# Kernel optimization log

Hardware: AMD Instinct MI355X
Metric: run time of the kernel (lower is better)

## Reference

```python
import jax, jax.numpy as jnp
import numpy as np

HEADS = 4
C_HEAD = 32


def setup_inputs() -> dict:
    key = jax.random.key(0)
    k1, k2, k3 = jax.random.split(key, 3)
    c_in = 256
    c_hid = HEADS * C_HEAD  # 128
    x = jax.random.normal(k1, (4, c_in, 64, 64), dtype=jnp.float32)
    # 1x1 conv weights stored as [out, in]
    w_qkv = jax.random.normal(k2, (3 * c_hid, c_in), dtype=jnp.float32) * (c_in ** -0.5)
    w_out = jax.random.normal(k3, (c_in, c_hid), dtype=jnp.float32) * (c_hid ** -0.5)
    b_out = jnp.zeros((c_in,), dtype=jnp.float32)
    return {"x": x, "w_qkv": w_qkv, "w_out": w_out, "b_out": b_out}


def reference(x, w_qkv, w_out, b_out):
    b, c, h, w = x.shape
    scale = C_HEAD ** -0.5
    # 1x1 conv == channel matmul
    qkv = jnp.einsum('bchw,oc->bohw', x, w_qkv)  # [b, 3*c_hid, h, w]
    q, k, v = jnp.split(qkv, 3, axis=1)
    # b (heads c_head) x y -> b heads c_head (x y)
    def to_heads(t):
        return t.reshape(b, HEADS, C_HEAD, h * w)
    q, k, v = to_heads(q) * scale, to_heads(k), to_heads(v)
    sim = jnp.einsum('bhci,bhcj->bhij', q, k)  # [b, heads, N, N]
    sim = sim - jax.lax.stop_gradient(jnp.max(sim, axis=-1, keepdims=True))
    attn = jax.nn.softmax(sim, axis=-1)
    out = jnp.einsum('bhij,bhcj->bhic', attn, v)  # [b, heads, N, c_head]
    # b h (x y) c -> b (h c) x y
    out = out.transpose(0, 1, 3, 2).reshape(b, HEADS * C_HEAD, h, w)
    out = jnp.einsum('bchw,oc->bohw', out, w_out) + b_out[None, :, None, None]
    return out
```

## Files before the change

kernel.cpp:

```cpp
#include <hip/hip_runtime.h>
#include <hip/hip_bf16.h>
#include <cstdint>
#include <cstddef>

#define NB 4
#define CIN 256
#define CHID 128
#define HEADS 4
#define CHEAD 32
#define NPOS 4096
#define BH 16
#define NTOT 16384
#define QKV_O 384
#define QSCALE_LOG2E 0.2550348229f

typedef float f32x4 __attribute__((ext_vector_type(4)));
typedef float f32x16 __attribute__((ext_vector_type(16)));
typedef short s16x8 __attribute__((ext_vector_type(8)));

static __device__ __forceinline__ unsigned short f2bf(float f) {
    union { float f; unsigned u; } v; v.f = f;
    unsigned r = v.u + 0x7FFFu + ((v.u >> 16) & 1u);
    return (unsigned short)(r >> 16);
}

static __device__ __forceinline__ unsigned int pk2bf(float a, float b) {
    union { __hip_bfloat162 h; unsigned int u; } c;
    c.h = __float22bfloat162_rn(float2{a, b});
    return c.u;
}

static __device__ __forceinline__ void plswap(unsigned& a, unsigned& b) {
#if __has_builtin(__builtin_amdgcn_permlane32_swap)
    auto r = __builtin_amdgcn_permlane32_swap((int)a, (int)b, false, false);
    a = (unsigned)r[0];
    b = (unsigned)r[1];
#else
    int hh = (threadIdx.x >> 5) & 1;
    unsigned ta = (unsigned)__shfl_xor((int)a, 32);
    unsigned tb = (unsigned)__shfl_xor((int)b, 32);
    unsigned na = hh ? tb : a;
    unsigned nb = hh ? b : ta;
    a = na; b = nb;
#endif
}

static __device__ __forceinline__ s16x8 mk8(unsigned a, unsigned b, unsigned c, unsigned d) {
    union { unsigned u[4]; s16x8 v; } x;
    x.u[0] = a; x.u[1] = b; x.u[2] = c; x.u[3] = d;
    return x.v;
}

static __device__ __forceinline__ void async_cp16(const void* g, void* l) {
    __builtin_amdgcn_global_load_lds((const __attribute__((address_space(1))) unsigned int*)g,
                                     (__attribute__((address_space(3))) unsigned int*)l, 16, 0, 0);
}

#define MFMA32(a, b, c) __builtin_amdgcn_mfma_f32_32x32x16_bf16(a, b, c, 0, 0, 0)

__global__ void k_convert_w(const float* __restrict__ wqkv, const float* __restrict__ wout,
                            unsigned short* __restrict__ wqkv_bf, unsigned short* __restrict__ wout_bf) {
    int i = blockIdx.x * 256 + threadIdx.x;
    if (i < QKV_O * CIN) wqkv_bf[i] = f2bf(wqkv[i]);
    if (i < CIN * CHID)  wout_bf[i]  = f2bf(wout[i]);
}

__global__ __launch_bounds__(256) void k_transpose_x(const float* __restrict__ x,
                                                     unsigned short* __restrict__ xT) {
    __shared__ float tile[32][33];
    const int ntiles = NPOS / 32;
    const int ctiles = CIN / 32;
    int b   = blockIdx.x / (ntiles * ctiles);
    int rem = blockIdx.x % (ntiles * ctiles);
    int ct = rem / ntiles;
    int nt = rem % ntiles;
    int c0 = ct * 32, n0 = nt * 32;
    int tc = threadIdx.x / 32;
    int tn = threadIdx.x % 32;
    const float* xb = x + (size_t)b * CIN * NPOS;
#pragma unroll
    for (int it = 0; it < 4; ++it) {
        int c = tc + it * 8;
        tile[c][tn] = xb[(size_t)(c0 + c) * NPOS + n0 + tn];
    }
    __syncthreads();
    unsigned short* xTb = xT + (size_t)b * NPOS * CIN;
#pragma unroll
    for (int it = 0; it < 4; ++it) {
        int n = tc + it * 8;
        xTb[(size_t)(n0 + n) * CIN + c0 + tn] = f2bf(tile[tn][n]);
    }
}

__global__ __launch_bounds__(256, 4) void k_qkv(const unsigned short* __restrict__ wq,
                                                const unsigned short* __restrict__ xT,
                                                unsigned short* __restrict__ Q,
                                                unsigned short* __restrict__ K,
                                                unsigned short* __restrict__ V) {
    __shared__ __align__(16) unsigned char smem[2 * 12288];
    int mt = blockIdx.x % 3;
    int nt = blockIdx.x / 3;
    int wid = threadIdx.x >> 6, lane = threadIdx.x & 63;
    int quad = lane >> 4, low4 = lane & 15;
    int o0 = mt * 128, n0 = nt * 64;
    int lb = lane * 16;

    const unsigned short* srcA0 = wq + (size_t)(o0 + wid * 32 + low4) * CIN + quad * 8;
    const unsigned short* srcA1 = srcA0 + 16 * CIN;
    const unsigned short* srcB  = xT + (size_t)(n0 + wid * 16 + low4) * CIN + quad * 8;
    int dA0 = wid * 2048, dA1 = dA0 + 1024, dB = 8192 + wid * 1024;

    async_cp16(srcA0, smem + dA0 + lb);
    async_cp16(srcA1, smem + dA1 + lb);
    async_cp16(srcB,  smem + dB  + lb);
    __syncthreads();

    f32x4 acc[2][4] = {};
    for (int c = 0; c < 8; ++c) {
        if (c < 7) {
            unsigned char* nxt = smem + ((c + 1) & 1) * 12288;
            async_cp16(srcA0 + (c + 1) * 32, nxt + dA0 + lb);
            async_cp16(srcA1 + (c + 1) * 32, nxt + dA1 + lb);
            async_cp16(srcB  + (c + 1) * 32, nxt + dB  + lb);
        }
        const unsigned char* cur = smem + (c & 1) * 12288;
        s16x8 a0 = *(const s16x8*)(cur + wid * 2048 + lb);
        s16x8 a1 = *(const s16x8*)(cur + wid * 2048 + 1024 + lb);
#pragma unroll
        for (int j = 0; j < 4; ++j) {
            s16x8 bj = *(const s16x8*)(cur + 8192 + j * 1024 + lb);
            acc[0][j] = __builtin_amdgcn_mfma_f32_16x16x32_bf16(a0, bj, acc[0][j], 0, 0, 0);
            acc[1][j] = __builtin_amdgcn_mfma_f32_16x16x32_bf16(a1, bj, acc[1][j], 0, 0, 0);
        }
        __syncthreads();
    }

#pragma unroll
    for (int i = 0; i < 2; ++i) {
        int ob = o0 + wid * 32 + i * 16 + quad * 4;
#pragma unroll
        for (int j = 0; j < 4; ++j) {
            int nG = n0 + j * 16 + low4;
            int b = nG >> 12, n = nG & 4095;
            f32x4 v = acc[i][j];
            if (ob < 128) {
                int head = ob >> 5, ch = ob & 31;
                unsigned long long d =
                    (unsigned long long)pk2bf(v[0] * QSCALE_LOG2E, v[1] * QSCALE_LOG2E) |
                    ((unsigned long long)pk2bf(v[2] * QSCALE_LOG2E, v[3] * QSCALE_LOG2E) << 32);
                *(unsigned long long*)(Q + ((size_t)(b * 4 + head) * NPOS + n) * 32 + ch) = d;
            } else if (ob < 256) {
                int o2 = ob - 128; int head = o2 >> 5, ch = o2 & 31;
                unsigned long long d =
                    (unsigned long long)pk2bf(v[0], v[1]) |
                    ((unsigned long long)pk2bf(v[2], v[3]) << 32);
                *(unsigned long long*)(K + ((size_t)(b * 4 + head) * NPOS + n) * 32 + ch) = d;
            } else {
#pragma unroll
                for (int r = 0; r < 4; ++r) {
                    int o2 = ob + r - 256; int head = o2 >> 5, ch = o2 & 31;
                    V[((size_t)((b * 4 + head) * 32 + ch)) * NPOS + n] = f2bf(v[r]);
                }
            }
        }
    }
}

__global__ __launch_bounds__(256, 2) void k_attn(const unsigned short* __restrict__ Q,
                                                 const unsigned short* __restrict__ K,
                                                 const unsigned short* __restrict__ V,
                                                 unsigned short* __restrict__ attnO) {
    __shared__ __align__(16) unsigned char smem[2 * 16384];
    int bh = blockIdx.x & 15;
    int qt = blockIdx.x >> 4;
    int wid = threadIdx.x >> 6, lane = threadIdx.x & 63;
    int q5 = lane & 31, h = lane >> 5;
    int qg = wid & 1, kh = wid >> 1;
    int q0 = qt * 128 + qg * 64;
    int khk = kh * 2048;

    const unsigned short* Qp  = Q + (size_t)bh * NPOS * 32;
    const unsigned short* Kbh = K + (size_t)bh * NPOS * 32;
    const unsigned short* Vbh = V + (size_t)bh * 32 * NPOS;

    s16x8 bq00 = *(const s16x8*)(Qp + (size_t)(q0 + q5) * 32 + h * 8);
    s16x8 bq01 = *(const s16x8*)(Qp + (size_t)(q0 + q5) * 32 + 16 + h * 8);
    s16x8 bq10 = *(const s16x8*)(Qp + (size_t)(q0 + 32 + q5) * 32 + h * 8);
    s16x8 bq11 = *(const s16x8*)(Qp + (size_t)(q0 + 32 + q5) * 32 + 16 + h * 8);

    const unsigned short* sK = Kbh + (size_t)q5 * 32 + h * 8;
    const unsigned short* sV = Vbh + (size_t)q5 * NPOS + h * 8;
    unsigned char* wbase0 = smem + kh * 8192;
    unsigned char* wbase1 = smem + 16384 + kh * 8192;

    auto stage = [&](int bufi, int k0) {
        unsigned char* wb = bufi ? wbase1 : wbase0;
        if (qg == 0) {
            const unsigned short* p = sK + (size_t)k0 * 32;
            async_cp16(p,        wb);
            async_cp16(p + 16,   wb + 1024);
            async_cp16(p + 1024, wb + 2048);
            async_cp16(p + 1040, wb + 3072);
        } else {
            const unsigned short* p = sV + k0;
            async_cp16(p,      wb + 4096);
            async_cp16(p + 16, wb + 5120);
            async_cp16(p + 32, wb + 6144);
            async_cp16(p + 48, wb + 7168);
        }
    };

    f32x16 oT0 = {}, oT1 = {};
    float lsum0 = 0.0f, lsum1 = 0.0f;
    const int lby = lane * 16;

    stage(0, khk);
    __syncthreads();

#pragma unroll 1
    for (int it = 0; it < 32; ++it) {
        if (it + 1 < 32) stage((it + 1) & 1, khk + (it + 1) * 64);
        const unsigned char* kb = smem + (it & 1) * 16384 + kh * 8192;
#pragma unroll
        for (int t = 0; t < 2; ++t) {
            s16x8 ak0 = *(const s16x8*)(kb + t * 2048 + lby);
            s16x8 ak1 = *(const s16x8*)(kb + t * 2048 + 1024 + lby);
            f32x16 s0 = {}, s1 = {};
            s0 = MFMA32(ak0, bq00, s0); s0 = MFMA32(ak1, bq01, s0);
            s1 = MFMA32(ak0, bq10, s1); s1 = MFMA32(ak1, bq11, s1);
            unsigned p0[8], p1[8];
#pragma unroll
            for (int i = 0; i < 8; ++i) {
                float a0 = __builtin_amdgcn_exp2f(s0[2 * i]);
                float a1 = __builtin_amdgcn_exp2f(s0[2 * i + 1]);
                float b0 = __builtin_amdgcn_exp2f(s1[2 * i]);
                float b1 = __builtin_amdgcn_exp2f(s1[2 * i + 1]);
                lsum0 += a0 + a1;
                lsum1 += b0 + b1;
                p0[i] = pk2bf(a0, a1);
                p1[i] = pk2bf(b0, b1);
            }
            plswap(p0[0], p0[2]); plswap(p0[1], p0[3]);
            plswap(p0[4], p0[6]); plswap(p0[5], p0[7]);
            plswap(p1[0], p1[2]); plswap(p1[1], p1[3]);
            plswap(p1[4], p1[6]); plswap(p1[5], p1[7]);
            s16x8 bp0lo = mk8(p0[0], p0[1], p0[2], p0[3]);
            s16x8 bp0hi = mk8(p0[4], p0[5], p0[6], p0[7]);
            s16x8 bp1lo = mk8(p1[0], p1[1], p1[2], p1[3]);
            s16x8 bp1hi = mk8(p1[4], p1[5], p1[6], p1[7]);

            s16x8 av0 = *(const s16x8*)(kb + 4096 + (2 * t) * 1024 + lby);
            s16x8 av1 = *(const s16x8*)(kb + 4096 + (2 * t + 1) * 1024 + lby);
            oT0 = MFMA32(av0, bp0lo, oT0); oT0 = MFMA32(av1, bp0hi, oT0);
            oT1 = MFMA32(av0, bp1lo, oT1); oT1 = MFMA32(av1, bp1hi, oT1);
        }
        __syncthreads();
    }

    lsum0 += __shfl_xor(lsum0, 32);
    lsum1 += __shfl_xor(lsum1, 32);

    float* area = (float*)smem + qg * 2176;
    if (kh) {
#pragma unroll
        for (int j = 0; j < 4; ++j) {
            *(f32x4*)(area + j * 256 + lane * 4) =
                f32x4{oT0[4 * j], oT0[4 * j + 1], oT0[4 * j + 2], oT0[4 * j + 3]};
            *(f32x4*)(area + 1024 + j * 256 + lane * 4) =
                f32x4{oT1[4 * j], oT1[4 * j + 1], oT1[4 * j + 2], oT1[4 * j + 3]};
        }
        area[2048 + lane * 2]     = lsum0;
        area[2048 + lane * 2 + 1] = lsum1;
    }
    __syncthreads();
    if (!kh) {
        lsum0 += area[2048 + lane * 2];
        lsum1 += area[2048 + lane * 2 + 1];
        float inv0 = 1.0f / lsum0, inv1 = 1.0f / lsum1;
        int b = bh >> 2, head = bh & 3;
        int n0 = q0 + q5, n1 = q0 + 32 + q5;
        unsigned short* base0 = attnO + ((size_t)(b * NPOS + n0)) * CHID + head * 32 + 4 * h;
        unsigned short* base1 = attnO + ((size_t)(b * NPOS + n1)) * CHID + head * 32 + 4 * h;
#pragma unroll
        for (int j = 0; j < 4; ++j) {
            f32x4 r0 = *(const f32x4*)(area + j * 256 + lane * 4);
            f32x4 r1 = *(const f32x4*)(area + 1024 + j * 256 + lane * 4);
            unsigned long long d0 =
                (unsigned long long)pk2bf((oT0[4 * j] + r0[0]) * inv0, (oT0[4 * j + 1] + r0[1]) * inv0) |
                ((unsigned long long)pk2bf((oT0[4 * j + 2] + r0[2]) * inv0, (oT0[4 * j + 3] + r0[3]) * inv0) << 32);
            *(unsigned long long*)(base0 + 8 * j) = d0;
            unsigned long long d1 =
                (unsigned long long)pk2bf((oT1[4 * j] + r1[0]) * inv1, (oT1[4 * j + 1] + r1[1]) * inv1) |
                ((unsigned long long)pk2bf((oT1[4 * j + 2] + r1[2]) * inv1, (oT1[4 * j + 3] + r1[3]) * inv1) << 32);
            *(unsigned long long*)(base1 + 8 * j) = d1;
        }
    }
}

__global__ __launch_bounds__(256, 4) void k_out(const unsigned short* __restrict__ wo,
                                                const unsigned short* __restrict__ attnO,
                                                const float* __restrict__ bias,
                                                float* __restrict__ out) {
    __shared__ __align__(16) unsigned char smem[2 * 12288];
    int mt = blockIdx.x & 1;
    int nt = blockIdx.x >> 1;
    int wid = threadIdx.x >> 6, lane = threadIdx.x & 63;
    int quad = lane >> 4, low4 = lane & 15;
    int o0 = mt * 128, n0 = nt * 64;
    int lb = lane * 16;

    const unsigned short* srcA0 = wo + (size_t)(o0 + wid * 32 + low4) * CHID + quad * 8;
    const unsigned short* srcA1 = srcA0 + 16 * CHID;
    const unsigned short* srcB  = attnO + (size_t)(n0 + wid * 16 + low4) * CHID + quad * 8;
    int dA0 = wid * 2048, dA1 = dA0 + 1024, dB = 8192 + wid * 1024;

    async_cp16(srcA0, smem + dA0 + lb);
    async_cp16(srcA1, smem + dA1 + lb);
    async_cp16(srcB,  smem + dB  + lb);
    __syncthreads();

    f32x4 acc[2][4] = {};
    for (int c = 0; c < 4; ++c) {
        if (c < 3) {
            unsigned char* nxt = smem + ((c + 1) & 1) * 12288;
            async_cp16(srcA0 + (c + 1) * 32, nxt + dA0 + lb);
            async_cp16(srcA1 + (c + 1) * 32, nxt + dA1 + lb);
            async_cp16(srcB  + (c + 1) * 32, nxt + dB  + lb);
        }
        const unsigned char* cur = smem + (c & 1) * 12288;
        s16x8 a0 = *(const s16x8*)(cur + wid * 2048 + lb);
        s16x8 a1 = *(const s16x8*)(cur + wid * 2048 + 1024 + lb);
#pragma unroll
        for (int j = 0; j < 4; ++j) {
            s16x8 bj = *(const s16x8*)(cur + 8192 + j * 1024 + lb);
            acc[0][j] = __builtin_amdgcn_mfma_f32_16x16x32_bf16(a0, bj, acc[0][j], 0, 0, 0);
            acc[1][j] = __builtin_amdgcn_mfma_f32_16x16x32_bf16(a1, bj, acc[1][j], 0, 0, 0);
        }
        __syncthreads();
    }

#pragma unroll
    for (int i = 0; i < 2; ++i) {
        int ob = o0 + wid * 32 + i * 16 + quad * 4;
#pragma unroll
        for (int j = 0; j < 4; ++j) {
            int nG = n0 + j * 16 + low4;
            int b = nG >> 12, n = nG & 4095;
#pragma unroll
            for (int r = 0; r < 4; ++r) {
                int o = ob + r;
                out[((size_t)(b * CIN + o)) * NPOS + n] = acc[i][j][r] + bias[o];
            }
        }
    }
}

extern "C" void kernel_launch(void* const* d_in, const int* in_sizes, int n_in,
                              void* d_out, int out_size, void* d_ws, size_t ws_size,
                              hipStream_t stream) {
    const float* x    = (const float*)d_in[0];
    const float* wqkv = (const float*)d_in[1];
    const float* wout = (const float*)d_in[2];
    const float* bout = (const float*)d_in[3];
    float* out = (float*)d_out;

    unsigned short* Q       = (unsigned short*)d_ws;
    unsigned short* K       = Q + (size_t)BH * NPOS * 32;
    unsigned short* V       = K + (size_t)BH * NPOS * 32;
    unsigned short* attnO   = V + (size_t)BH * 32 * NPOS;
    unsigned short* xT      = attnO + (size_t)NTOT * CHID;
    unsigned short* wqkv_bf = xT + (size_t)NTOT * CIN;
    unsigned short* wout_bf = wqkv_bf + QKV_O * CIN;

    k_convert_w<<<(QKV_O * CIN + 255) / 256, 256, 0, stream>>>(wqkv, wout, wqkv_bf, wout_bf);
    k_transpose_x<<<NB * (CIN / 32) * (NPOS / 32), 256, 0, stream>>>(x, xT);
    k_qkv<<<3 * (NTOT / 64), 256, 0, stream>>>(wqkv_bf, xT, Q, K, V);
    k_attn<<<(NPOS / 128) * BH, 256, 0, stream>>>(Q, K, V, attnO);
    k_out<<<2 * (NTOT / 64), 256, 0, stream>>>(wout_bf, attnO, bout, out);
}
```

Baseline: 153.6 us.

## Split attention keys across more waves, fuse prep kernels, stage V stores via LDS

The attention kernel now launches 512 threads per block, so the key range is split four ways instead of two. The partial outputs from the extra waves are reduced through a larger 64KB shared buffer. The weight conversion and x transpose are merged into one launch, and the V-tile stores in the qkv kernel are transposed through LDS so they can be written as coalesced 16-byte vectors. The row-sum accumulator is also split into two chains to shorten the dependency. The trade-offs are a larger LDS footprint per attention block, which may cap occupancy, and an extra cross-wave reduction step.

```diff
diff --git a/kernel.cpp b/kernel.cpp
--- a/kernel.cpp
+++ b/kernel.cpp
@@ -58,15 +58,19 @@
 
 #define MFMA32(a, b, c) __builtin_amdgcn_mfma_f32_32x32x16_bf16(a, b, c, 0, 0, 0)
 
-__global__ void k_convert_w(const float* __restrict__ wqkv, const float* __restrict__ wout,
-                            unsigned short* __restrict__ wqkv_bf, unsigned short* __restrict__ wout_bf) {
-    int i = blockIdx.x * 256 + threadIdx.x;
-    if (i < QKV_O * CIN) wqkv_bf[i] = f2bf(wqkv[i]);
-    if (i < CIN * CHID)  wout_bf[i]  = f2bf(wout[i]);
-}
-
-__global__ __launch_bounds__(256) void k_transpose_x(const float* __restrict__ x,
-                                                     unsigned short* __restrict__ xT) {
+#define TBLOCKS (NB * (CIN / 32) * (NPOS / 32))
+__global__ __launch_bounds__(256) void k_prep(const float* __restrict__ x,
+                                              unsigned short* __restrict__ xT,
+                                              const float* __restrict__ wqkv,
+                                              const float* __restrict__ wout,
+                                              unsigned short* __restrict__ wqkv_bf,
+                                              unsigned short* __restrict__ wout_bf) {
+    if (blockIdx.x >= TBLOCKS) {
+        int i = (blockIdx.x - TBLOCKS) * 256 + threadIdx.x;
+        if (i < QKV_O * CIN) wqkv_bf[i] = f2bf(wqkv[i]);
+        if (i < CIN * CHID)  wout_bf[i] = f2bf(wout[i]);
+        return;
+    }
     __shared__ float tile[32][33];
     const int ntiles = NPOS / 32;
     const int ctiles = CIN / 32;
@@ -135,49 +139,62 @@
         __syncthreads();
     }
 
-#pragma unroll
-    for (int i = 0; i < 2; ++i) {
-        int ob = o0 + wid * 32 + i * 16 + quad * 4;
-#pragma unroll
-        for (int j = 0; j < 4; ++j) {
-            int nG = n0 + j * 16 + low4;
-            int b = nG >> 12, n = nG & 4095;
-            f32x4 v = acc[i][j];
-            if (ob < 128) {
-                int head = ob >> 5, ch = ob & 31;
+    if (mt < 2) {
+        unsigned short* dst = (mt == 0) ? Q : K;
+        float sc = (mt == 0) ? QSCALE_LOG2E : 1.0f;
+#pragma unroll
+        for (int i = 0; i < 2; ++i) {
+            int ol = wid * 32 + i * 16 + quad * 4;
+            int head = ol >> 5, ch = ol & 31;
+#pragma unroll
+            for (int j = 0; j < 4; ++j) {
+                int nG = n0 + j * 16 + low4;
+                int b = nG >> 12, n = nG & 4095;
+                f32x4 v = acc[i][j];
                 unsigned long long d =
-                    (unsigned long long)pk2bf(v[0] * QSCALE_LOG2E, v[1] * QSCALE_LOG2E) |
-                    ((unsigned long long)pk2bf(v[2] * QSCALE_LOG2E, v[3] * QSCALE_LOG2E) << 32);
-                *(unsigned long long*)(Q + ((size_t)(b * 4 + head) * NPOS + n) * 32 + ch) = d;
-            } else if (ob < 256) {
-                int o2 = ob - 128; int head = o2 >> 5, ch = o2 & 31;
-                unsigned long long d =
-                    (unsigned long long)pk2bf(v[0], v[1]) |
-                    ((unsigned long long)pk2bf(v[2], v[3]) << 32);
-                *(unsigned long long*)(K + ((size_t)(b * 4 + head) * NPOS + n) * 32 + ch) = d;
-            } else {
-#pragma unroll
-                for (int r = 0; r < 4; ++r) {
-                    int o2 = ob + r - 256; int head = o2 >> 5, ch = o2 & 31;
-                    V[((size_t)((b * 4 + head) * 32 + ch)) * NPOS + n] = f2bf(v[r]);
-                }
+                    (unsigned long long)pk2bf(v[0] * sc, v[1] * sc) |
+                    ((unsigned long long)pk2bf(v[2] * sc, v[3] * sc) << 32);
+                *(unsigned long long*)(dst + ((size_t)(b * 4 + head) * NPOS + n) * 32 + ch) = d;
             }
         }
-    }
-}
-
-__global__ __launch_bounds__(256, 2) void k_attn(const unsigned short* __restrict__ Q,
+    } else {
+        unsigned short* vt = (unsigned short*)smem;
+#pragma unroll
+        for (int i = 0; i < 2; ++i) {
+            int ol = wid * 32 + i * 16 + quad * 4;
+#pragma unroll
+            for (int j = 0; j < 4; ++j) {
+                int col = j * 16 + low4;
+#pragma unroll
+                for (int r = 0; r < 4; ++r) vt[(ol + r) * 80 + col] = f2bf(acc[i][j][r]);
+            }
+        }
+        __syncthreads();
+        int b = n0 >> 12, nbase = n0 & 4095;
+#pragma unroll
+        for (int rep = 0; rep < 4; ++rep) {
+            int idx = rep * 256 + threadIdx.x;
+            int row = idx >> 3, c8 = idx & 7;
+            s16x8 val = *(const s16x8*)(vt + row * 80 + c8 * 8);
+            int head = row >> 5, ch = row & 31;
+            *(s16x8*)(V + ((size_t)((b * 4 + head) * 32 + ch)) * NPOS + nbase + c8 * 8) = val;
+        }
+    }
+}
+
+__global__ __launch_bounds__(512, 4) void k_attn(const unsigned short* __restrict__ Q,
                                                  const unsigned short* __restrict__ K,
                                                  const unsigned short* __restrict__ V,
                                                  unsigned short* __restrict__ attnO) {
-    __shared__ __align__(16) unsigned char smem[2 * 16384];
+    __shared__ __align__(16) unsigned char smem[65536];
     int bh = blockIdx.x & 15;
     int qt = blockIdx.x >> 4;
-    int wid = threadIdx.x >> 6, lane = threadIdx.x & 63;
+    int wid = threadIdx.x >> 6;
+    int lane = threadIdx.x & 63;
     int q5 = lane & 31, h = lane >> 5;
     int qg = wid & 1, kh = wid >> 1;
     int q0 = qt * 128 + qg * 64;
-    int khk = kh * 2048;
+    int khk = kh * 1024;
 
     const unsigned short* Qp  = Q + (size_t)bh * NPOS * 32;
     const unsigned short* Kbh = K + (size_t)bh * NPOS * 32;
@@ -190,11 +207,9 @@
 
     const unsigned short* sK = Kbh + (size_t)q5 * 32 + h * 8;
     const unsigned short* sV = Vbh + (size_t)q5 * NPOS + h * 8;
-    unsigned char* wbase0 = smem + kh * 8192;
-    unsigned char* wbase1 = smem + 16384 + kh * 8192;
 
     auto stage = [&](int bufi, int k0) {
-        unsigned char* wb = bufi ? wbase1 : wbase0;
+        unsigned char* wb = smem + bufi * 32768 + kh * 8192;
         if (qg == 0) {
             const unsigned short* p = sK + (size_t)k0 * 32;
             async_cp16(p,        wb);
@@ -211,16 +226,16 @@
     };
 
     f32x16 oT0 = {}, oT1 = {};
-    float lsum0 = 0.0f, lsum1 = 0.0f;
+    float l0a = 0.0f, l0b = 0.0f, l1a = 0.0f, l1b = 0.0f;
     const int lby = lane * 16;
 
     stage(0, khk);
     __syncthreads();
 
 #pragma unroll 1
-    for (int it = 0; it < 32; ++it) {
-        if (it + 1 < 32) stage((it + 1) & 1, khk + (it + 1) * 64);
-        const unsigned char* kb = smem + (it & 1) * 16384 + kh * 8192;
+    for (int it = 0; it < 16; ++it) {
+        if (it + 1 < 16) stage((it + 1) & 1, khk + (it + 1) * 64);
+        const unsigned char* kb = smem + (it & 1) * 32768 + kh * 8192;
 #pragma unroll
         for (int t = 0; t < 2; ++t) {
             s16x8 ak0 = *(const s16x8*)(kb + t * 2048 + lby);
@@ -235,8 +250,8 @@
                 float a1 = __builtin_amdgcn_exp2f(s0[2 * i + 1]);
                 float b0 = __builtin_amdgcn_exp2f(s1[2 * i]);
                 float b1 = __builtin_amdgcn_exp2f(s1[2 * i + 1]);
-                lsum0 += a0 + a1;
-                lsum1 += b0 + b1;
+                if (i & 1) { l0a += a0 + a1; l1a += b0 + b1; }
+                else       { l0b += a0 + a1; l1b += b0 + b1; }
                 p0[i] = pk2bf(a0, a1);
                 p1[i] = pk2bf(b0, b1);
             }
@@ -257,11 +272,12 @@
         __syncthreads();
     }
 
+    float lsum0 = l0a + l0b, lsum1 = l1a + l1b;
     lsum0 += __shfl_xor(lsum0, 32);
     lsum1 += __shfl_xor(lsum1, 32);
 
-    float* area = (float*)smem + qg * 2176;
     if (kh) {
+        float* area = (float*)(smem + ((kh - 1) * 2 + qg) * 8704);
 #pragma unroll
         for (int j = 0; j < 4; ++j) {
             *(f32x4*)(area + j * 256 + lane * 4) =
@@ -274,24 +290,36 @@
     }
     __syncthreads();
     if (!kh) {
-        lsum0 += area[2048 + lane * 2];
-        lsum1 += area[2048 + lane * 2 + 1];
+#pragma unroll
+        for (int m = 0; m < 3; ++m) {
+            const float* area = (const float*)(smem + (m * 2 + qg) * 8704);
+#pragma unroll
+            for (int j = 0; j < 4; ++j) {
+                f32x4 r0 = *(const f32x4*)(area + j * 256 + lane * 4);
+                f32x4 r1 = *(const f32x4*)(area + 1024 + j * 256 + lane * 4);
+#pragma unroll
+                for (int i = 0; i < 4; ++i) {
+                    oT0[4 * j + i] += r0[i];
+                    oT1[4 * j + i] += r1[i];
+                }
+            }
+            lsum0 += area[2048 + lane * 2];
+            lsum1 += area[2048 + lane * 2 + 1];
+        }
         float inv0 = 1.0f / lsum0, inv1 = 1.0f / lsum1;
         int b = bh >> 2, head = bh & 3;
-        int n0 = q0 + q5, n1 = q0 + 32 + q5;
-        unsigned short* base0 = attnO + ((size_t)(b * NPOS + n0)) * CHID + head * 32 + 4 * h;
-        unsigned short* base1 = attnO + ((size_t)(b * NPOS + n1)) * CHID + head * 32 + 4 * h;
+        int n0q = q0 + q5, n1q = q0 + 32 + q5;
+        unsigned short* base0 = attnO + ((size_t)(b * NPOS + n0q)) * CHID + head * 32 + 4 * h;
+        unsigned short* base1 = attnO + ((size_t)(b * NPOS + n1q)) * CHID + head * 32 + 4 * h;
 #pragma unroll
         for (int j = 0; j < 4; ++j) {
-            f32x4 r0 = *(const f32x4*)(area + j * 256 + lane * 4);
-            f32x4 r1 = *(const f32x4*)(area + 1024 + j * 256 + lane * 4);
             unsigned long long d0 =
-                (unsigned long long)pk2bf((oT0[4 * j] + r0[0]) * inv0, (oT0[4 * j + 1] + r0[1]) * inv0) |
-                ((unsigned long long)pk2bf((oT0[4 * j + 2] + r0[2]) * inv0, (oT0[4 * j + 3] + r0[3]) * inv0) << 32);
+                (unsigned long long)pk2bf(oT0[4 * j] * inv0, oT0[4 * j + 1] * inv0) |
+                ((unsigned long long)pk2bf(oT0[4 * j + 2] * inv0, oT0[4 * j + 3] * inv0) << 32);
             *(unsigned long long*)(base0 + 8 * j) = d0;
             unsigned long long d1 =
-                (unsigned long long)pk2bf((oT1[4 * j] + r1[0]) * inv1, (oT1[4 * j + 1] + r1[1]) * inv1) |
-                ((unsigned long long)pk2bf((oT1[4 * j + 2] + r1[2]) * inv1, (oT1[4 * j + 3] + r1[3]) * inv1) << 32);
+                (unsigned long long)pk2bf(oT1[4 * j] * inv1, oT1[4 * j + 1] * inv1) |
+                ((unsigned long long)pk2bf(oT1[4 * j + 2] * inv1, oT1[4 * j + 3] * inv1) << 32);
             *(unsigned long long*)(base1 + 8 * j) = d1;
         }
     }
@@ -372,9 +400,8 @@
     unsigned short* wqkv_bf = xT + (size_t)NTOT * CIN;
     unsigned short* wout_bf = wqkv_bf + QKV_O * CIN;
 
-    k_convert_w<<<(QKV_O * CIN + 255) / 256, 256, 0, stream>>>(wqkv, wout, wqkv_bf, wout_bf);
-    k_transpose_x<<<NB * (CIN / 32) * (NPOS / 32), 256, 0, stream>>>(x, xT);
+    k_prep<<<TBLOCKS + (QKV_O * CIN + 255) / 256, 256, 0, stream>>>(x, xT, wqkv, wout, wqkv_bf, wout_bf);
     k_qkv<<<3 * (NTOT / 64), 256, 0, stream>>>(wqkv_bf, xT, Q, K, V);
-    k_attn<<<(NPOS / 128) * BH, 256, 0, stream>>>(Q, K, V, attnO);
+    k_attn<<<(NPOS / 128) * BH, 512, 0, stream>>>(Q, K, V, attnO);
     k_out<<<2 * (NTOT / 64), 256, 0, stream>>>(wout_bf, attnO, bout, out);
 }
```

After: 204.5 us. +33.1%, slower.
